# Performance work log

Hardware: AMD Instinct MI355X
Metric: run time of the kernel (lower is better)

## Reference

```python
import itertools
import jax, jax.numpy as jnp
import numpy as np

# ---- JPEG constants (match utils.y_table / utils.c_table) ----
_Y_TABLE = np.array([
    [16, 11, 10, 16, 24, 40, 51, 61],
    [12, 12, 14, 19, 26, 58, 60, 55],
    [14, 13, 16, 24, 40, 57, 69, 56],
    [14, 17, 22, 29, 51, 87, 80, 62],
    [18, 22, 37, 56, 68, 109, 103, 77],
    [24, 35, 55, 64, 81, 104, 113, 92],
    [49, 64, 78, 87, 103, 121, 120, 101],
    [72, 92, 95, 98, 112, 100, 103, 99]], dtype=np.float32)
_C_TABLE = np.full((8, 8), 99, dtype=np.float32)
_C_TABLE[:4, :4] = np.array([[17, 18, 24, 47], [18, 21, 26, 66],
                             [24, 26, 56, 99], [47, 66, 99, 99]], dtype=np.float32)

# RGB -> YCbCr matrix (code defines M then uses M.T via tensordot dims=1)
_YCBCR_M = np.array([[0.299, 0.587, 0.114],
                     [-0.168736, -0.331264, 0.5],
                     [0.5, -0.418688, -0.081312]], dtype=np.float32)
_SHIFT = np.array([0.0, 128.0, 128.0], dtype=np.float32)

_cx = np.cos((2 * np.arange(8)[:, None] + 1) * np.arange(8)[None, :] * np.pi / 16)  # [x,u]
_DCT = np.einsum('xu,yv->xyuv', _cx, _cx).astype(np.float32)
_alpha = np.array([1.0 / np.sqrt(2)] + [1.0] * 7)
_DCT_SCALE = (np.outer(_alpha, _alpha) * 0.25).astype(np.float32)

FACTOR = 1.0
K = 8  # block size


def _block_split(x):
    # x: [B, H, W] -> [B, H*W/64, 8, 8]
    B, H, W = x.shape
    x = x.reshape(B, H // K, K, W // K, K)
    x = jnp.transpose(x, (0, 1, 3, 2, 4))
    return x.reshape(B, -1, K, K)


def _dct_8x8(x):
    # x: [B, N, 8, 8]
    x = x - 128.0
    return jnp.asarray(_DCT_SCALE) * jnp.einsum('bnxy,xyuv->bnuv', x, jnp.asarray(_DCT))


def _avg_pool2(x):
    # 2x2 average pooling, stride 2; x: [B, H, W]
    B, H, W = x.shape
    return x.reshape(B, H // 2, 2, W // 2, 2).mean(axis=(2, 4))


def _compress(image):
    # image: [B, 3, H, W] in [0, 1]
    img = jnp.transpose(image * 255.0, (0, 2, 3, 1))  # [B, H, W, 3]
    ycbcr = jnp.einsum('bhwc,cd->bhwd', img, jnp.asarray(_YCBCR_M.T)) + jnp.asarray(_SHIFT)
    y = ycbcr[..., 0]
    cb = _avg_pool2(ycbcr[..., 1])
    cr = _avg_pool2(ycbcr[..., 2])
    y_q = jnp.round(_dct_8x8(_block_split(y)) / (jnp.asarray(_Y_TABLE) * FACTOR))
    cb_q = jnp.round(_dct_8x8(_block_split(cb)) / (jnp.asarray(_C_TABLE) * FACTOR))
    cr_q = jnp.round(_dct_8x8(_block_split(cr)) / (jnp.asarray(_C_TABLE) * FACTOR))
    return y_q, cb_q, cr_q


def setup_inputs() -> dict:
    key = jax.random.key(0)
    image = jax.random.uniform(key, (32, 3, 512, 512), dtype=jnp.float32)
    return {"image": image}


def reference(image):
    return _compress(image)
```

## Files before the change

kernel.cpp:

```cpp
#include <hip/hip_runtime.h>
#include <cmath>


namespace jc {

constexpr double c1 = 0.98078528040323044912618223613424;
constexpr double c2 = 0.92387953251128675612818318939679;
constexpr double c3 = 0.83146961230254523707878837761791;
constexpr double c4 = 0.70710678118654752440084436210485;
constexpr double c5 = 0.55557023301960222474283081394853;
constexpr double c6 = 0.38268343236508977172845998403040;
constexpr double c7 = 0.19509032201612826784828486847702;
constexpr double alpha0 = 0.70710678118654746171979706919384;

struct Tab {
  float tt[4096];
  float sc[64];
  float yq[64];
  float cq[64];
  constexpr Tab() : tt(), sc(), yq(), cq() {
    const double CX[8][8] = {
      {1.0,  c1,  c2,  c3,  c4,  c5,  c6,  c7},
      {1.0,  c3,  c6, -c7, -c4, -c1, -c2, -c5},
      {1.0,  c5, -c6, -c1, -c4,  c7,  c2,  c3},
      {1.0,  c7, -c2, -c5,  c4,  c3, -c6, -c1},
      {1.0, -c7, -c2,  c5,  c4, -c3, -c6,  c1},
      {1.0, -c5, -c6,  c1, -c4, -c7,  c2, -c3},
      {1.0, -c3,  c6,  c7, -c4,  c1, -c2,  c5},
      {1.0, -c1,  c2, -c3,  c4, -c5,  c6, -c7}};
    for (int i = 0; i < 64; ++i) {
      const int u = i >> 3, v = i & 7;
      for (int j = 0; j < 64; ++j) {
        const int x = j >> 3, y = j & 7;
        tt[j * 64 + i] = (float)(CX[x][u] * CX[y][v]);
      }
      const double au = (u == 0) ? alpha0 : 1.0;
      const double av = (v == 0) ? alpha0 : 1.0;
      sc[i] = (float)((au * av) * 0.25);
    }
    const int YT[64] = {
      16, 11, 10, 16, 24, 40, 51, 61,
      12, 12, 14, 19, 26, 58, 60, 55,
      14, 13, 16, 24, 40, 57, 69, 56,
      14, 17, 22, 29, 51, 87, 80, 62,
      18, 22, 37, 56, 68, 109, 103, 77,
      24, 35, 55, 64, 81, 104, 113, 92,
      49, 64, 78, 87, 103, 121, 120, 101,
      72, 92, 95, 98, 112, 100, 103, 99};
    const int CT[64] = {
      17, 18, 24, 47, 99, 99, 99, 99,
      18, 21, 26, 66, 99, 99, 99, 99,
      24, 26, 56, 99, 99, 99, 99, 99,
      47, 66, 99, 99, 99, 99, 99, 99,
      99, 99, 99, 99, 99, 99, 99, 99,
      99, 99, 99, 99, 99, 99, 99, 99,
      99, 99, 99, 99, 99, 99, 99, 99,
      99, 99, 99, 99, 99, 99, 99, 99};
    for (int i = 0; i < 64; ++i) {
      yq[i] = (float)YT[i];
      cq[i] = (float)CT[i];
    }
  }
};

__device__ constexpr Tab TT;

}

__device__ __forceinline__ float vmul(float a, float b) {
  float r; asm("v_mul_f32 %0, %1, %2" : "=v"(r) : "v"(a), "v"(b)); return r;
}
__device__ __forceinline__ float vadd(float a, float b) {
  float r; asm("v_add_f32 %0, %1, %2" : "=v"(r) : "v"(a), "v"(b)); return r;
}
__device__ __forceinline__ float vsubf(float a, float b) {
  float r; asm("v_sub_f32 %0, %1, %2" : "=v"(r) : "v"(a), "v"(b)); return r;
}

__device__ __forceinline__ float chro_t(float tR, float tG, float tB,
                                        float kR, float kG, float kB) {
  float a = vmul(tR, kR);
  a = vadd(a, vmul(tG, kG));
  a = vadd(a, vmul(tB, kB));
  return vadd(a, 128.0f);
}

__global__ __launch_bounds__(256, 4) void jpeg_kernel(const float* __restrict__ img,
                                                      float* __restrict__ out) {
  __shared__ float Xs[96][68];

  const int wid = blockIdx.x;
  const int t = threadIdx.x;
  const int b = wid >> 6;
  const int r = wid & 63;

  {
    const int yb = t & 63;
    const int q = t >> 6;
    const int by = yb >> 3, bx = yb & 7;
    const int prow = (r >> 3) * 64 + by * 8 + 2 * q;
    const int pcol = (r & 7) * 64 + bx * 8;
    const float* rp = img + (size_t)b * 786432 + (size_t)prow * 512 + pcol;

    float tv[3][2][8];
#pragma unroll
    for (int c = 0; c < 3; ++c) {
#pragma unroll
      for (int rr = 0; rr < 2; ++rr) {
        const float* p0 = rp + c * 262144 + rr * 512;
        const float4 va = *(const float4*)(p0);
        const float4 vb = *(const float4*)(p0 + 4);
        tv[c][rr][0] = vmul(va.x, 255.0f);
        tv[c][rr][1] = vmul(va.y, 255.0f);
        tv[c][rr][2] = vmul(va.z, 255.0f);
        tv[c][rr][3] = vmul(va.w, 255.0f);
        tv[c][rr][4] = vmul(vb.x, 255.0f);
        tv[c][rr][5] = vmul(vb.y, 255.0f);
        tv[c][rr][6] = vmul(vb.z, 255.0f);
        tv[c][rr][7] = vmul(vb.w, 255.0f);
      }
    }
#pragma unroll
    for (int rr = 0; rr < 2; ++rr) {
#pragma unroll
      for (int y = 0; y < 8; ++y) {
        float a = vmul(tv[0][rr][y], 0.299f);
        a = vadd(a, vmul(tv[1][rr][y], 0.587f));
        a = vadd(a, vmul(tv[2][rr][y], 0.114f));
        Xs[yb][16 * q + rr * 8 + y] = vsubf(a, 128.0f);
      }
    }
    const int lcr = 4 * by + q;
#pragma unroll
    for (int pc = 0; pc < 4; ++pc) {
      const int lcc = 4 * bx + pc;
      const int crow = 64 + ((lcr >> 3) * 4 + (lcc >> 3));
      const int cell = (lcr & 7) * 8 + (lcc & 7);
      const int e = 2 * pc, o = 2 * pc + 1;
      {
        const float p00 = chro_t(tv[0][0][e], tv[1][0][e], tv[2][0][e], -0.168736f, -0.331264f, 0.5f);
        const float p01 = chro_t(tv[0][0][o], tv[1][0][o], tv[2][0][o], -0.168736f, -0.331264f, 0.5f);
        const float p10 = chro_t(tv[0][1][e], tv[1][1][e], tv[2][1][e], -0.168736f, -0.331264f, 0.5f);
        const float p11 = chro_t(tv[0][1][o], tv[1][1][o], tv[2][1][o], -0.168736f, -0.331264f, 0.5f);
        const float s = vadd(vadd(vadd(p00, p01), p10), p11);
        Xs[crow][cell] = vsubf(vmul(s, 0.25f), 128.0f);
      }
      {
        const float p00 = chro_t(tv[0][0][e], tv[1][0][e], tv[2][0][e], 0.5f, -0.418688f, -0.081312f);
        const float p01 = chro_t(tv[0][0][o], tv[1][0][o], tv[2][0][o], 0.5f, -0.418688f, -0.081312f);
        const float p10 = chro_t(tv[0][1][e], tv[1][1][e], tv[2][1][e], 0.5f, -0.418688f, -0.081312f);
        const float p11 = chro_t(tv[0][1][o], tv[1][1][o], tv[2][1][o], 0.5f, -0.418688f, -0.081312f);
        const float s = vadd(vadd(vadd(p00, p01), p10), p11);
        Xs[crow + 16][cell] = vsubf(vmul(s, 0.25f), 128.0f);
      }
    }
  }

  const int w = t >> 6;
  const int lane = t & 63;
  float T[64];
#pragma unroll
  for (int j = 0; j < 64; ++j) T[j] = jc::TT.tt[j * 64 + lane];
  const float scv = jc::TT.sc[lane];
  const float yqv = jc::TT.yq[lane];
  const float cqv = jc::TT.cq[lane];

  __syncthreads();

  const int ybase = b * 4096 + (r >> 3) * 512 + (r & 7) * 8;
  const int cbase = b * 1024 + (r >> 3) * 128 + (r & 7) * 4;

  auto emit = [&](int blk, float acc) {
    float qv;
    size_t off;
    if (blk < 64) {
      qv = yqv;
      off = ((size_t)(ybase + (blk >> 3) * 64 + (blk & 7))) << 6;
    } else {
      qv = cqv;
      const int cc = blk & 15;
      off = (size_t)8388608 + (blk >= 80 ? (size_t)2097152 : (size_t)0) +
            (((size_t)(cbase + (cc >> 2) * 32 + (cc & 3))) << 6);
    }
    out[off + lane] = rintf(__fdiv_rn(vmul(scv, acc), qv));
  };

  for (int n = 0; n < 24; n += 2) {
    const int bA = w * 24 + n;
    const int bB = bA + 1;
    float a0 = 0.0f, a1 = 0.0f;
#pragma unroll
    for (int j4 = 0; j4 < 16; ++j4) {
      const float4 xA = *(const float4*)&Xs[bA][j4 * 4];
      const float4 xB = *(const float4*)&Xs[bB][j4 * 4];
      a0 = vadd(a0, vmul(T[4 * j4 + 0], xA.x));
      a1 = vadd(a1, vmul(T[4 * j4 + 0], xB.x));
      a0 = vadd(a0, vmul(T[4 * j4 + 1], xA.y));
      a1 = vadd(a1, vmul(T[4 * j4 + 1], xB.y));
      a0 = vadd(a0, vmul(T[4 * j4 + 2], xA.z));
      a1 = vadd(a1, vmul(T[4 * j4 + 2], xB.z));
      a0 = vadd(a0, vmul(T[4 * j4 + 3], xA.w));
      a1 = vadd(a1, vmul(T[4 * j4 + 3], xB.w));
    }
    emit(bA, a0);
    emit(bB, a1);
  }
}

extern "C" void kernel_launch(void* const* d_in, const int* in_sizes, int n_in,
                              void* d_out, int out_size, void* d_ws, size_t ws_size,
                              hipStream_t stream) {
  (void)in_sizes; (void)n_in; (void)d_ws; (void)ws_size; (void)out_size;
  const float* img = (const float*)d_in[0];
  float* out = (float*)d_out;
  jpeg_kernel<<<dim3(2048), dim3(256), 0, stream>>>(img, out);
}
```

Before: 183.8 us.

## Restructure DCT stage: lane-per-block packed math with SGPR basis and LDS-staged vector stores

Each lane now holds one block's 64 pixels in registers, and the DCT basis coefficients are read as wave-uniform scalar constants feeding v_pk_mul/v_pk_add packed FP32 math. Before, each lane kept one output coefficient's basis column in 64 VGPRs and re-read block rows from LDS. Quantised results go into a shared output tile and are written back as float4 stores instead of scalar per-lane stores. The aim is to halve the VALU instruction count and widen global stores. In exchange, the chroma waves leave half their lanes idle, and the change adds extra barriers and more scalar-memory traffic for the basis table.

```diff
diff --git a/kernel.cpp b/kernel.cpp
--- a/kernel.cpp
+++ b/kernel.cpp
@@ -1,6 +1,8 @@
 #include <hip/hip_runtime.h>
 #include <cmath>
 
+
+typedef float f2 __attribute__((ext_vector_type(2)));
 
 namespace jc {
 
@@ -14,11 +16,11 @@
 constexpr double alpha0 = 0.70710678118654746171979706919384;
 
 struct Tab {
-  float tt[4096];
+  alignas(16) float tq4[16384];
   float sc[64];
   float yq[64];
   float cq[64];
-  constexpr Tab() : tt(), sc(), yq(), cq() {
+  constexpr Tab() : tq4(), sc(), yq(), cq() {
     const double CX[8][8] = {
       {1.0,  c1,  c2,  c3,  c4,  c5,  c6,  c7},
       {1.0,  c3,  c6, -c7, -c4, -c1, -c2, -c5},
@@ -28,12 +30,18 @@
       {1.0, -c5, -c6,  c1, -c4, -c7,  c2, -c3},
       {1.0, -c3,  c6,  c7, -c4,  c1, -c2,  c5},
       {1.0, -c1,  c2, -c3,  c4, -c5,  c6, -c7}};
+    for (int q = 0; q < 16; ++q) {
+      for (int j = 0; j < 64; ++j) {
+        const int x = j >> 3, y = j & 7;
+        const int is[4] = {q, q + 32, q + 16, q + 48};
+        for (int m = 0; m < 4; ++m) {
+          const int u = is[m] >> 3, v = is[m] & 7;
+          tq4[(q * 64 + j) * 4 + m] = (float)(CX[x][u] * CX[y][v]);
+        }
+      }
+    }
     for (int i = 0; i < 64; ++i) {
       const int u = i >> 3, v = i & 7;
-      for (int j = 0; j < 64; ++j) {
-        const int x = j >> 3, y = j & 7;
-        tt[j * 64 + i] = (float)(CX[x][u] * CX[y][v]);
-      }
       const double au = (u == 0) ? alpha0 : 1.0;
       const double av = (v == 0) ? alpha0 : 1.0;
       sc[i] = (float)((au * av) * 0.25);
@@ -76,6 +84,20 @@
 __device__ __forceinline__ float vsubf(float a, float b) {
   float r; asm("v_sub_f32 %0, %1, %2" : "=v"(r) : "v"(a), "v"(b)); return r;
 }
+__device__ __forceinline__ float vmul_sv(float su, float v) {
+  float r; asm("v_mul_f32 %0, %1, %2" : "=v"(r) : "s"(su), "v"(v)); return r;
+}
+__device__ __forceinline__ f2 pk_mul_lo(f2 tp, f2 x) {
+  f2 r; asm("v_pk_mul_f32 %0, %1, %2 op_sel:[0,0] op_sel_hi:[1,0]"
+            : "=v"(r) : "s"(tp), "v"(x)); return r;
+}
+__device__ __forceinline__ f2 pk_mul_hi(f2 tp, f2 x) {
+  f2 r; asm("v_pk_mul_f32 %0, %1, %2 op_sel:[0,1] op_sel_hi:[1,1]"
+            : "=v"(r) : "s"(tp), "v"(x)); return r;
+}
+__device__ __forceinline__ f2 pk_add(f2 a, f2 b) {
+  f2 r; asm("v_pk_add_f32 %0, %1, %2" : "=v"(r) : "v"(a), "v"(b)); return r;
+}
 
 __device__ __forceinline__ float chro_t(float tR, float tG, float tB,
                                         float kR, float kG, float kB) {
@@ -87,7 +109,8 @@
 
 __global__ __launch_bounds__(256, 4) void jpeg_kernel(const float* __restrict__ img,
                                                       float* __restrict__ out) {
-  __shared__ float Xs[96][68];
+  __shared__ float Xs[96][65];
+  __shared__ float Os[96][36];
 
   const int wid = blockIdx.x;
   const int t = threadIdx.x;
@@ -156,54 +179,86 @@
     }
   }
 
-  const int w = t >> 6;
+  __syncthreads();
+
+  const int w = __builtin_amdgcn_readfirstlane(t >> 6);
   const int lane = t & 63;
-  float T[64];
-#pragma unroll
-  for (int j = 0; j < 64; ++j) T[j] = jc::TT.tt[j * 64 + lane];
-  const float scv = jc::TT.sc[lane];
-  const float yqv = jc::TT.yq[lane];
-  const float cqv = jc::TT.cq[lane];
-
-  __syncthreads();
-
-  const int ybase = b * 4096 + (r >> 3) * 512 + (r & 7) * 8;
-  const int cbase = b * 1024 + (r >> 3) * 128 + (r & 7) * 4;
-
-  auto emit = [&](int blk, float acc) {
-    float qv;
-    size_t off;
-    if (blk < 64) {
-      qv = yqv;
-      off = ((size_t)(ybase + (blk >> 3) * 64 + (blk & 7))) << 6;
-    } else {
-      qv = cqv;
-      const int cc = blk & 15;
-      off = (size_t)8388608 + (blk >= 80 ? (size_t)2097152 : (size_t)0) +
-            (((size_t)(cbase + (cc >> 2) * 32 + (cc & 3))) << 6);
-    }
-    out[off + lane] = rintf(__fdiv_rn(vmul(scv, acc), qv));
-  };
-
-  for (int n = 0; n < 24; n += 2) {
-    const int bA = w * 24 + n;
-    const int bB = bA + 1;
-    float a0 = 0.0f, a1 = 0.0f;
-#pragma unroll
-    for (int j4 = 0; j4 < 16; ++j4) {
-      const float4 xA = *(const float4*)&Xs[bA][j4 * 4];
-      const float4 xB = *(const float4*)&Xs[bB][j4 * 4];
-      a0 = vadd(a0, vmul(T[4 * j4 + 0], xA.x));
-      a1 = vadd(a1, vmul(T[4 * j4 + 0], xB.x));
-      a0 = vadd(a0, vmul(T[4 * j4 + 1], xA.y));
-      a1 = vadd(a1, vmul(T[4 * j4 + 1], xB.y));
-      a0 = vadd(a0, vmul(T[4 * j4 + 2], xA.z));
-      a1 = vadd(a1, vmul(T[4 * j4 + 2], xB.z));
-      a0 = vadd(a0, vmul(T[4 * j4 + 3], xA.w));
-      a1 = vadd(a1, vmul(T[4 * j4 + 3], xB.w));
-    }
-    emit(bA, a0);
-    emit(bB, a1);
+  const int g = w & 1;
+  const bool isY = (w < 2);
+  const int Bl = isY ? lane : (64 + (lane & 31));
+  const bool active = isY || (lane < 32);
+
+  f2 X2[32];
+  {
+    const float* xr = Xs[Bl];
+#pragma unroll
+    for (int p = 0; p < 32; ++p) {
+      f2 v;
+      v.x = xr[2 * p];
+      v.y = xr[2 * p + 1];
+      X2[p] = v;
+    }
+  }
+
+  const float* qt = isY ? jc::TT.yq : jc::TT.cq;
+
+  const int ry = r >> 3, rx = r & 7;
+  const int ybase = b * 4096 + ry * 512 + rx * 8;
+  const int cbase = b * 1024 + ry * 128 + rx * 4;
+
+#pragma unroll
+  for (int rnd = 0; rnd < 2; ++rnd) {
+#pragma unroll
+    for (int c = 0; c < 4; ++c) {
+      const int q = 8 * g + 4 * rnd + c;
+      const float4* tq = (const float4*)&jc::TT.tq4[q * 256];
+      f2 aA = {0.0f, 0.0f};
+      f2 aB = {0.0f, 0.0f};
+#pragma unroll
+      for (int j = 0; j < 64; j += 2) {
+        const float4 t0 = tq[j];
+        const float4 t1 = tq[j + 1];
+        const f2 x = X2[j >> 1];
+        const f2 t0a = {t0.x, t0.y};
+        const f2 t0b = {t0.z, t0.w};
+        const f2 t1a = {t1.x, t1.y};
+        const f2 t1b = {t1.z, t1.w};
+        aA = pk_add(aA, pk_mul_lo(t0a, x));
+        aB = pk_add(aB, pk_mul_lo(t0b, x));
+        aA = pk_add(aA, pk_mul_hi(t1a, x));
+        aB = pk_add(aB, pk_mul_hi(t1b, x));
+      }
+      if (active) {
+        const int col = 4 * g + c;
+        Os[Bl][col]      = rintf(__fdiv_rn(vmul_sv(jc::TT.sc[q],      aA.x), qt[q]));
+        Os[Bl][8 + col]  = rintf(__fdiv_rn(vmul_sv(jc::TT.sc[q + 16], aB.x), qt[q + 16]));
+        Os[Bl][16 + col] = rintf(__fdiv_rn(vmul_sv(jc::TT.sc[q + 32], aA.y), qt[q + 32]));
+        Os[Bl][24 + col] = rintf(__fdiv_rn(vmul_sv(jc::TT.sc[q + 48], aB.y), qt[q + 48]));
+      }
+    }
+
+    __syncthreads();
+
+#pragma unroll
+    for (int s = 0; s < 3; ++s) {
+      const int idx = t + 256 * s;
+      const int bb = idx >> 3;
+      const int s4 = idx & 7;
+      const float4 v = *(const float4*)&Os[bb][4 * s4];
+      const int i0 = 16 * (s4 >> 1) + 8 * (s4 & 1) + 4 * rnd;
+      size_t base;
+      if (bb < 64) {
+        base = ((size_t)(ybase + (bb >> 3) * 64 + (bb & 7))) << 6;
+      } else {
+        const int typ = (bb >= 80);
+        const int cb = bb - 64 - 16 * typ;
+        base = (size_t)8388608 + (size_t)typ * 2097152 +
+               (((size_t)(cbase + (cb >> 2) * 32 + (cb & 3))) << 6);
+      }
+      *(float4*)(out + base + i0) = v;
+    }
+
+    __syncthreads();
   }
 }
 
```

Result: slower. 221.0 us (+20.2%).
